# Optimization experiments

Hardware: AMD Instinct MI355X
Metric: run time of the kernel (lower is better)

## Reference

```python
import jax, jax.numpy as jnp
import numpy as np
from jax import lax

PALETTE = 256


def setup_inputs() -> dict:
    key = jax.random.key(0)
    k1, k2, k3, k4 = jax.random.split(key, 4)
    x = jax.random.normal(k1, (16, 64, 256, 256), dtype=jnp.float32)
    lookup_table = jax.random.normal(k2, (PALETTE,), dtype=jnp.float32) * 0.05
    weight_idx = jax.random.randint(k3, (64, 64, 3, 3), 0, PALETTE, dtype=jnp.int32)
    bias = jax.random.normal(k4, (64,), dtype=jnp.float32) * 0.01
    return {"x": x, "lookup_table": lookup_table, "weight_idx": weight_idx, "bias": bias}


def reference(x, lookup_table, weight_idx, bias):
    # Dequantize: palette gather produces full OIHW weight tensor.
    full_w = lookup_table[weight_idx]  # [O, I, kH, kW] float32
    # conv2d with stride=1, padding=0 (hardcoded in module), dilation=1, groups=1
    out = lax.conv_general_dilated(
        x, full_w,
        window_strides=(1, 1),
        padding='VALID',
        rhs_dilation=(1, 1),
        dimension_numbers=('NCHW', 'OIHW', 'NCHW'),
        feature_group_count=1,
    )
    return out + bias[None, :, None, None]
```

## Files before the change

kernel.cpp:

```cpp
#include <hip/hip_runtime.h>


typedef __bf16 bf16x8 __attribute__((ext_vector_type(8)));
typedef float f32x4 __attribute__((ext_vector_type(4)));

union Frag {
    uint4 q;
    bf16x8 v;
};

__global__ __launch_bounds__(256) void dequant_B(
        const float* __restrict__ lut, const int* __restrict__ widx,
        uint4* __restrict__ Bws) {
    int s = blockIdx.x * 256 + threadIdx.x;
    int l = s & 63;
    int nt = (s >> 6) & 3;
    int kc = s >> 8;
    if (kc >= 18) return;
    int r = kc >> 1;
    int kh = r / 3, kw = r - kh * 3;
    int o = nt * 16 + (l & 15);
    int c0 = (kc & 1) * 32 + (l >> 4) * 8;
    Frag f;
#pragma unroll
    for (int j = 0; j < 8; ++j) {
        int c = c0 + j;
        int idx = widx[((o * 64 + c) * 3 + kh) * 3 + kw];
        f.v[j] = (__bf16)lut[idx];
    }
    Bws[s] = f.q;
}

#define LDS_PIX 266

__global__ __launch_bounds__(256, 4) void conv_mfma(
        const float* __restrict__ x, const float* __restrict__ bias,
        const uint4* __restrict__ Bws, float* __restrict__ out) {
    __shared__ uint4 ldsA[4 * LDS_PIX];

    int bx = blockIdx.x;
    int ow0 = (bx & 3) * 64;
    int oh0 = ((bx >> 2) & 127) * 2;
    int n = bx >> 9;
    int t = threadIdx.x;

    const float* xn = x + (size_t)n * (64 * 256 * 256);

    int w = t >> 6;
    int l = t & 63;
    int l15 = l & 15, l4 = l >> 4;
    int ohl = w >> 1;
    int owb = (w & 1) * 32;

    int st_col = t & 63;
    int st_cb  = t >> 6;
    int tl_cb  = t & 3;
    int tl_rc  = t >> 2;
    int tl_rr  = tl_rc >> 1;
    int tl_col = 64 + (tl_rc & 1);
    int tl_xc  = ow0 + tl_col; if (tl_xc > 255) tl_xc = 255;

    f32x4 acc[2][4] = {};

    for (int h = 0; h < 2; ++h) {
        {
            const float* sb = xn + (h * 4 + st_cb) * (8 * 65536) + ow0 + st_col;
#pragma unroll
            for (int rr = 0; rr < 4; ++rr) {
                int y = oh0 + rr; if (y > 255) y = 255;
                const float* src = sb + y * 256;
                Frag f;
#pragma unroll
                for (int j = 0; j < 8; ++j)
                    f.v[j] = (__bf16)src[j * 65536];
                ldsA[st_cb * LDS_PIX + rr * 66 + st_col] = f.q;
            }
            if (t < 32) {
                int y = oh0 + tl_rr; if (y > 255) y = 255;
                const float* src = xn + (h * 4 + tl_cb) * (8 * 65536) + y * 256 + tl_xc;
                Frag f;
#pragma unroll
                for (int j = 0; j < 8; ++j)
                    f.v[j] = (__bf16)src[j * 65536];
                ldsA[tl_cb * LDS_PIX + tl_rr * 66 + tl_col] = f.q;
            }
        }
        __syncthreads();

#pragma unroll
        for (int i = 0; i < 9; ++i) {
            int kh = i / 3, kw = i - kh * 3;
            int kc = 2 * i + h;
            int pix = (ohl + kh) * 66 + owb + l15 + kw;

            Frag b[4];
#pragma unroll
            for (int nt = 0; nt < 4; ++nt)
                b[nt].q = Bws[(kc * 4 + nt) * 64 + l];

            Frag a[2];
#pragma unroll
            for (int mt = 0; mt < 2; ++mt)
                a[mt].q = ldsA[l4 * LDS_PIX + pix + mt * 16];

#pragma unroll
            for (int mt = 0; mt < 2; ++mt)
#pragma unroll
                for (int nt = 0; nt < 4; ++nt)
                    acc[mt][nt] = __builtin_amdgcn_mfma_f32_16x16x32_bf16(
                        a[mt].v, b[nt].v, acc[mt][nt], 0, 0, 0);
        }
        if (h == 0) __syncthreads();
    }

    int oh = oh0 + ohl;
    if (oh < 254) {
#pragma unroll
        for (int nt = 0; nt < 4; ++nt) {
            int o = nt * 16 + l15;
            float bv = bias[o];
            float* obase = out + (((size_t)n * 64 + o) * 254 + oh) * 254 + ow0;
#pragma unroll
            for (int mt = 0; mt < 2; ++mt) {
#pragma unroll
                for (int rg = 0; rg < 4; ++rg) {
                    int owl = owb + mt * 16 + l4 * 4 + rg;
                    if (ow0 + owl < 254)
                        obase[owl] = acc[mt][nt][rg] + bv;
                }
            }
        }
    }
}

extern "C" void kernel_launch(void* const* d_in, const int* in_sizes, int n_in,
                              void* d_out, int out_size, void* d_ws, size_t ws_size,
                              hipStream_t stream) {
    const float* x    = (const float*)d_in[0];
    const float* lut  = (const float*)d_in[1];
    const int*   widx = (const int*)d_in[2];
    const float* bias = (const float*)d_in[3];
    float* out = (float*)d_out;
    uint4* Bws = (uint4*)d_ws;

    dequant_B<<<18, 256, 0, stream>>>(lut, widx, Bws);
    conv_mfma<<<8192, 256, 0, stream>>>(x, bias, (const uint4*)Bws, out);
}
```

Baseline: 564.0 us.

## Widen conv tile to 128 columns, vectorize input loads, stage output through LDS

Each block now covers 128 output columns by 2 rows, and each wave computes 8 M-tiles by 2 N-tiles, so each A fragment is reused across more MFMAs. The grid is resized to 127 row pairs so no block is spent on out-of-range rows. Input staging uses float4 global loads and packs channel pairs into 32-bit LDS writes, replacing scalar strided loads. The epilogue transposes accumulators through LDS so each lane writes contiguous float2 runs per output channel. In exchange the kernel uses more LDS and more accumulator registers, which may lower occupancy and add LDS bank conflicts.

```diff
diff --git a/kernel.cpp b/kernel.cpp
--- a/kernel.cpp
+++ b/kernel.cpp
@@ -3,6 +3,7 @@
 
 typedef __bf16 bf16x8 __attribute__((ext_vector_type(8)));
 typedef float f32x4 __attribute__((ext_vector_type(4)));
+typedef float f32x2 __attribute__((ext_vector_type(2)));
 
 union Frag {
     uint4 q;
@@ -31,17 +32,21 @@
     Bws[s] = f.q;
 }
 
-#define LDS_PIX 266
+#define A_CB 530
 
 __global__ __launch_bounds__(256, 4) void conv_mfma(
         const float* __restrict__ x, const float* __restrict__ bias,
         const uint4* __restrict__ Bws, float* __restrict__ out) {
-    __shared__ uint4 ldsA[4 * LDS_PIX];
+    __shared__ uint4 ldsA[4 * A_CB];
+    unsigned* lds32 = (unsigned*)ldsA;
 
     int bx = blockIdx.x;
-    int ow0 = (bx & 3) * 64;
-    int oh0 = ((bx >> 2) & 127) * 2;
-    int n = bx >> 9;
+    int owt = bx & 1;
+    int rem = bx >> 1;
+    int ohp = rem % 127;
+    int n   = rem / 127;
+    int ow0 = owt * 128;
+    int oh0 = ohp * 2;
     int t = threadIdx.x;
 
     const float* xn = x + (size_t)n * (64 * 256 * 256);
@@ -49,40 +54,52 @@
     int w = t >> 6;
     int l = t & 63;
     int l15 = l & 15, l4 = l >> 4;
-    int ohl = w >> 1;
-    int owb = (w & 1) * 32;
 
-    int st_col = t & 63;
-    int st_cb  = t >> 6;
     int tl_cb  = t & 3;
     int tl_rc  = t >> 2;
     int tl_rr  = tl_rc >> 1;
-    int tl_col = 64 + (tl_rc & 1);
+    int tl_col = 128 + (tl_rc & 1);
     int tl_xc  = ow0 + tl_col; if (tl_xc > 255) tl_xc = 255;
 
-    f32x4 acc[2][4] = {};
+    int ohl = w >> 1;
+    int ob  = (w & 1) * 2;
+
+    f32x4 acc[8][2] = {};
 
     for (int h = 0; h < 2; ++h) {
         {
-            const float* sb = xn + (h * 4 + st_cb) * (8 * 65536) + ow0 + st_col;
+            const float* cbase = xn + (size_t)(((h * 4 + w) * 8 + l4 * 2)) * 65536
+                                 + ow0;
 #pragma unroll
-            for (int rr = 0; rr < 4; ++rr) {
-                int y = oh0 + rr; if (y > 255) y = 255;
-                const float* src = sb + y * 256;
+            for (int ch2 = 0; ch2 < 2; ++ch2) {
+                const float* pb = cbase + ch2 * 64 + l15 * 4;
+                f32x4 f0[4], f1[4];
+#pragma unroll
+                for (int rr = 0; rr < 4; ++rr) {
+                    const float* p = pb + (oh0 + rr) * 256;
+                    f0[rr] = *(const f32x4*)(p);
+                    f1[rr] = *(const f32x4*)(p + 65536);
+                }
+#pragma unroll
+                for (int rr = 0; rr < 4; ++rr) {
+                    int gbase = w * A_CB + rr * 132 + ch2 * 64 + l15 * 4;
+#pragma unroll
+                    for (int i = 0; i < 4; ++i) {
+                        union { __bf16 hh[2]; unsigned u; } bp;
+                        bp.hh[0] = (__bf16)f0[rr][i];
+                        bp.hh[1] = (__bf16)f1[rr][i];
+                        lds32[(gbase + i) * 4 + l4] = bp.u;
+                    }
+                }
+            }
+            if (t < 32) {
+                const float* src = xn + (size_t)((h * 4 + tl_cb) * 8) * 65536
+                                   + (oh0 + tl_rr) * 256 + tl_xc;
                 Frag f;
 #pragma unroll
                 for (int j = 0; j < 8; ++j)
                     f.v[j] = (__bf16)src[j * 65536];
-                ldsA[st_cb * LDS_PIX + rr * 66 + st_col] = f.q;
-            }
-            if (t < 32) {
-                int y = oh0 + tl_rr; if (y > 255) y = 255;
-                const float* src = xn + (h * 4 + tl_cb) * (8 * 65536) + y * 256 + tl_xc;
-                Frag f;
-#pragma unroll
-                for (int j = 0; j < 8; ++j)
-                    f.v[j] = (__bf16)src[j * 65536];
-                ldsA[tl_cb * LDS_PIX + tl_rr * 66 + tl_col] = f.q;
+                ldsA[tl_cb * A_CB + tl_rr * 132 + tl_col] = f.q;
             }
         }
         __syncthreads();
@@ -91,44 +108,48 @@
         for (int i = 0; i < 9; ++i) {
             int kh = i / 3, kw = i - kh * 3;
             int kc = 2 * i + h;
-            int pix = (ohl + kh) * 66 + owb + l15 + kw;
 
-            Frag b[4];
+            Frag b[2];
 #pragma unroll
-            for (int nt = 0; nt < 4; ++nt)
-                b[nt].q = Bws[(kc * 4 + nt) * 64 + l];
+            for (int nt = 0; nt < 2; ++nt)
+                b[nt].q = Bws[(kc * 4 + ob + nt) * 64 + l];
 
-            Frag a[2];
+            Frag a[8];
 #pragma unroll
-            for (int mt = 0; mt < 2; ++mt)
-                a[mt].q = ldsA[l4 * LDS_PIX + pix + mt * 16];
+            for (int mt = 0; mt < 8; ++mt)
+                a[mt].q = ldsA[l4 * A_CB + (ohl + kh) * 132 + l15 + kw + mt * 16];
 
 #pragma unroll
-            for (int mt = 0; mt < 2; ++mt)
+            for (int mt = 0; mt < 8; ++mt)
 #pragma unroll
-                for (int nt = 0; nt < 4; ++nt)
+                for (int nt = 0; nt < 2; ++nt)
                     acc[mt][nt] = __builtin_amdgcn_mfma_f32_16x16x32_bf16(
                         a[mt].v, b[nt].v, acc[mt][nt], 0, 0, 0);
         }
-        if (h == 0) __syncthreads();
+        __syncthreads();
     }
 
+    float* slab = (float*)ldsA + w * (16 * 130);
+    int oseg = (w & 1) * 32;
     int oh = oh0 + ohl;
-    if (oh < 254) {
+    float* orow = out + ((size_t)n * 64 * 254 + oh) * 254 + ow0;
+    bool ok = (ow0 + l * 2 + 1) < 254;
 #pragma unroll
-        for (int nt = 0; nt < 4; ++nt) {
-            int o = nt * 16 + l15;
+    for (int nt = 0; nt < 2; ++nt) {
+#pragma unroll
+        for (int mt = 0; mt < 8; ++mt)
+#pragma unroll
+            for (int rg = 0; rg < 4; ++rg)
+                slab[l15 * 130 + mt * 16 + l4 * 4 + rg] = acc[mt][nt][rg];
+#pragma unroll
+        for (int j = 0; j < 16; ++j) {
+            int o = oseg + nt * 16 + j;
             float bv = bias[o];
-            float* obase = out + (((size_t)n * 64 + o) * 254 + oh) * 254 + ow0;
-#pragma unroll
-            for (int mt = 0; mt < 2; ++mt) {
-#pragma unroll
-                for (int rg = 0; rg < 4; ++rg) {
-                    int owl = owb + mt * 16 + l4 * 4 + rg;
-                    if (ow0 + owl < 254)
-                        obase[owl] = acc[mt][nt][rg] + bv;
-                }
-            }
+            f32x2 v;
+            v[0] = slab[j * 130 + l * 2]     + bv;
+            v[1] = slab[j * 130 + l * 2 + 1] + bv;
+            if (ok)
+                *(f32x2*)(orow + (size_t)o * (254 * 254) + l * 2) = v;
         }
     }
 }
@@ -144,5 +165,5 @@
     uint4* Bws = (uint4*)d_ws;
 
     dequant_B<<<18, 256, 0, stream>>>(lut, widx, Bws);
-    conv_mfma<<<8192, 256, 0, stream>>>(x, bias, (const uint4*)Bws, out);
+    conv_mfma<<<16 * 127 * 2, 256, 0, stream>>>(x, bias, (const uint4*)Bws, out);
 }
```

Measured after the change: 490.9 us. -13.0%, faster.
